# Kernel optimization log

Measured on AMD Instinct MI355X. Metric: run time of the kernel, lower is better.

The kernel has to match this reference:

```python
import jax, jax.numpy as jnp
import numpy as np

B, N, F, A = 8, 2048, 512, 512  # batch, n_dim (tokens), feature_dim, attention_dim
BN_EPS = 1e-5


def setup_inputs() -> dict:
    key = jax.random.key(0)
    ks = jax.random.split(key, 9)
    s_f = 1.0 / np.sqrt(F)
    s_a = 1.0 / np.sqrt(A)
    return {
        "x": jax.random.normal(ks[0], (B, N, F), dtype=jnp.float32),
        "Wq": jax.random.uniform(ks[1], (A, F), jnp.float32, -s_f, s_f),
        "bq": jax.random.uniform(ks[2], (A,), jnp.float32, -s_f, s_f),
        "Wk": jax.random.uniform(ks[3], (A, F), jnp.float32, -s_f, s_f),
        "bk": jax.random.uniform(ks[4], (A,), jnp.float32, -s_f, s_f),
        "Wv": jax.random.uniform(ks[5], (A, F), jnp.float32, -s_f, s_f),
        "bv": jax.random.uniform(ks[6], (A,), jnp.float32, -s_f, s_f),
        "Wo": jax.random.uniform(ks[7], (F, A), jnp.float32, -s_a, s_a),
        "bo": jax.random.uniform(ks[8], (F,), jnp.float32, -s_a, s_a),
        "gamma": jnp.ones((N,), dtype=jnp.float32),
        "beta": jnp.zeros((N,), dtype=jnp.float32),
    }


def reference(x, Wq, bq, Wk, bk, Wv, bv, Wo, bo, gamma, beta):
    # QKV projections: [B,N,F] -> [B,N,A]
    q = jnp.einsum("bnf,af->bna", x, Wq) + bq
    k = jnp.einsum("bnf,af->bna", x, Wk) + bk
    v = jnp.einsum("bnf,af->bna", x, Wv) + bv
    # unscaled single-head attention (no 1/sqrt(d) factor, matches source)
    scores = jnp.einsum("bna,bma->bnm", q, k)          # [B,N,N]
    weights = jax.nn.softmax(scores, axis=-1)
    feature = jnp.einsum("bnm,bma->bna", weights, v)    # [B,N,A]
    # LBR: Linear -> BatchNorm1d(n_dim) over channel dim N -> ReLU
    lin = jnp.einsum("bna,fa->bnf", feature, Wo) + bo   # [B,N,F]
    mean = jnp.mean(lin, axis=(0, 2), keepdims=True)    # stats over batch+last dim
    var = jnp.mean(jnp.square(lin - mean), axis=(0, 2), keepdims=True)  # biased var
    bn = gamma[None, :, None] * (lin - mean) * jax.lax.rsqrt(var + BN_EPS) + beta[None, :, None]
    return jax.nn.relu(bn) + x
```

## Files before the change

### kernel.cpp

```cpp
#include <hip/hip_runtime.h>
#include <hip/hip_fp16.h>
#include <stdint.h>

#define B_   8
#define N_   2048
#define F_   512
#define A_   512
#define MTOT (B_ * N_)

typedef unsigned short u16;
typedef unsigned int   u32;
typedef __attribute__((ext_vector_type(8))) __bf16    bf16x8;
typedef __attribute__((ext_vector_type(8))) _Float16  f16x8;
typedef __attribute__((ext_vector_type(4))) float     f32x4;

__device__ __forceinline__ u16 f2bf(float f) {
    u32 u = __builtin_bit_cast(u32, f);
    u32 r = u + 0x7fffu + ((u >> 16) & 1u);
    return (u16)(r >> 16);
}
__device__ __forceinline__ u16 f2h(float f) {
    _Float16 h = (_Float16)f;
    return __builtin_bit_cast(u16, h);
}

__device__ __forceinline__ void gload_lds16(const u16* g, u16* l) {
    __builtin_amdgcn_global_load_lds(
        (const __attribute__((address_space(1))) u32*)(const u32*)g,
        (__attribute__((address_space(3))) u32*)(u32*)l,
        16, 0, 0);
}

#define VMCNT(n) asm volatile("s_waitcnt vmcnt(" #n ")" ::: "memory")

__device__ __forceinline__ void sync_pre() {
    __builtin_amdgcn_sched_barrier(0);
    __builtin_amdgcn_s_barrier();
    asm volatile("s_waitcnt lgkmcnt(0)" ::: "memory");
    __builtin_amdgcn_sched_barrier(0);
}
__device__ __forceinline__ void sync_post() {
    __builtin_amdgcn_sched_barrier(0);
    __builtin_amdgcn_s_barrier();
}

template <int FMT>
__global__ __launch_bounds__(256) void cvt16(const float* __restrict__ in,
                                             u16* __restrict__ out, int n4) {
    int i = blockIdx.x * 256 + threadIdx.x;
    if (i >= n4) return;
    float4 v = ((const float4*)in)[i];
    u32 a, b;
    if constexpr (FMT == 0) {
        a = (u32)f2bf(v.x) | ((u32)f2bf(v.y) << 16);
        b = (u32)f2bf(v.z) | ((u32)f2bf(v.w) << 16);
    } else {
        a = (u32)f2h(v.x) | ((u32)f2h(v.y) << 16);
        b = (u32)f2h(v.z) | ((u32)f2h(v.w) << 16);
    }
    ((uint2*)out)[i] = make_uint2(a, b);
}

template <int BN, int BIAS_MODE, int OUT_FMT, int IN_FMT>
__global__ __launch_bounds__(512, 2)
void gemm8(const u16* __restrict__ A, int lda, long sA,
           const u16* __restrict__ Bm, int ldb, long sB,
           const float* __restrict__ bias,
           void* __restrict__ Cv, int ldc, long sC, int K, int bdiag)
{
    constexpr int UNITS = (BN == 256) ? 4 : 3;
    constexpr int NF = BN / 64;
    __shared__ alignas(16) u16 lds[2 * UNITS * 8192];

    const int z  = blockIdx.z;
    const int m0 = blockIdx.x * 256;
    const int n0 = blockIdx.y * BN;
    const u16* Ag = A  + (long)z * sA + (long)m0 * lda;
    const u16* Bg = Bm + (long)z * sB + (long)n0 * ldb + (long)(m0 >> 11) * bdiag;

    const int t = threadIdx.x;
    const int lane = t & 63;
    const int wave = t >> 6;
    const int wm = wave >> 2, wn = wave & 3;
    const int frow = lane & 15;
    const int fk8 = (lane >> 4) * 8;

    const int srr = t >> 3;
    const int ses = ((t & 7) * 8) ^ ((srr & 7) << 3);

    auto stageA = [&](int buf, int h, int kt) {
        u16* dst = &lds[(buf * UNITS + h) * 8192 + t * 8];
        const u16* g = Ag + kt * 64 + ses;
        gload_lds16(g + (long)(srr + h * 64) * lda,        dst);
        gload_lds16(g + (long)(srr + 128 + h * 64) * lda,  dst + 4096);
    };
    auto stageB = [&](int buf, int h, int kt) {
        u16* dst = &lds[(buf * UNITS + 2 + h) * 8192 + t * 8];
        const u16* g = Bg + kt * 64 + ses;
        int R0;
        if constexpr (BN == 256) R0 = (srr & 31) + ((srr >> 5) << 6) + h * 32;
        else                     R0 = srr;
        int R1 = R0 + ((BN == 256) ? 128 : 64);
        gload_lds16(g + (long)R0 * ldb, dst);
        gload_lds16(g + (long)R1 * ldb, dst + 4096);
    };
    auto rdA = [&](int buf, int q, int i, int ks) -> uint4 {
        int rr = wm * 64 + i * 16 + frow;
        int e  = (ks * 32 + fk8) ^ ((rr & 7) << 3);
        return *(const uint4*)&lds[(buf * UNITS + q) * 8192 + rr * 64 + e];
    };
    auto rdB = [&](int buf, int p, int j, int ks) -> uint4 {
        int rr = wn * 32 + j * 16 + frow;
        int e  = (ks * 32 + fk8) ^ ((rr & 7) << 3);
        return *(const uint4*)&lds[(buf * UNITS + 2 + p) * 8192 + rr * 64 + e];
    };
    auto MF = [&](uint4 a, uint4 b, f32x4 c) -> f32x4 {
        if constexpr (IN_FMT == 0)
            return __builtin_amdgcn_mfma_f32_16x16x32_bf16(
                __builtin_bit_cast(bf16x8, a), __builtin_bit_cast(bf16x8, b), c, 0, 0, 0);
        else
            return __builtin_amdgcn_mfma_f32_16x16x32_f16(
                __builtin_bit_cast(f16x8, a), __builtin_bit_cast(f16x8, b), c, 0, 0, 0);
    };

    f32x4 acc[8][NF];
#pragma unroll
    for (int i = 0; i < 8; i++)
#pragma unroll
        for (int j = 0; j < NF; j++)
#pragma unroll
            for (int r = 0; r < 4; r++) acc[i][j][r] = 0.f;

    uint4 fa[4][2], fb0[2][2], fb1[2][2];
    const int NT = K >> 6;

    if constexpr (BN == 256) {
        stageA(0, 0, 0); stageB(0, 0, 0); stageB(0, 1, 0); stageA(0, 1, 0);
        VMCNT(4);
    } else {
        stageA(0, 0, 0); stageB(0, 0, 0); stageA(0, 1, 0);
        VMCNT(2);
    }
    __builtin_amdgcn_sched_barrier(0);
    __builtin_amdgcn_s_barrier();

    for (int kt = 0; kt < NT; ++kt) {
        const int buf = kt & 1, nb = buf ^ 1;
        const bool st = (kt + 1 < NT);

        if constexpr (BN == 256) {
#pragma unroll
            for (int i = 0; i < 4; i++) { fa[i][0] = rdA(buf, 0, i, 0); fa[i][1] = rdA(buf, 0, i, 1); }
#pragma unroll
            for (int j = 0; j < 2; j++) { fb0[j][0] = rdB(buf, 0, j, 0); fb0[j][1] = rdB(buf, 0, j, 1); }
            if (st) { stageA(nb, 0, kt + 1); VMCNT(4); } else VMCNT(2);
            sync_pre();
            __builtin_amdgcn_s_setprio(1);
#pragma unroll
            for (int ks = 0; ks < 2; ks++)
#pragma unroll
                for (int i = 0; i < 4; i++)
#pragma unroll
                    for (int j = 0; j < 2; j++)
                        acc[i][j] = MF(fa[i][ks], fb0[j][ks], acc[i][j]);
            __builtin_amdgcn_s_setprio(0);
            sync_post();
#pragma unroll
            for (int j = 0; j < 2; j++) { fb1[j][0] = rdB(buf, 1, j, 0); fb1[j][1] = rdB(buf, 1, j, 1); }
            if (st) { stageB(nb, 0, kt + 1); VMCNT(4); } else VMCNT(0);
            sync_pre();
            __builtin_amdgcn_s_setprio(1);
#pragma unroll
            for (int ks = 0; ks < 2; ks++)
#pragma unroll
                for (int i = 0; i < 4; i++)
#pragma unroll
                    for (int j = 0; j < 2; j++)
                        acc[i][2 + j] = MF(fa[i][ks], fb1[j][ks], acc[i][2 + j]);
            __builtin_amdgcn_s_setprio(0);
            sync_post();
#pragma unroll
            for (int i = 0; i < 4; i++) { fa[i][0] = rdA(buf, 1, i, 0); fa[i][1] = rdA(buf, 1, i, 1); }
            if (st) stageB(nb, 1, kt + 1);
            sync_pre();
            __builtin_amdgcn_s_setprio(1);
#pragma unroll
            for (int ks = 0; ks < 2; ks++)
#pragma unroll
                for (int i = 0; i < 4; i++)
#pragma unroll
                    for (int j = 0; j < 2; j++)
                        acc[4 + i][j] = MF(fa[i][ks], fb0[j][ks], acc[4 + i][j]);
            __builtin_amdgcn_s_setprio(0);
            sync_post();
            if (st) { stageA(nb, 1, kt + 1); VMCNT(4); }
            sync_pre();
            __builtin_amdgcn_s_setprio(1);
#pragma unroll
            for (int ks = 0; ks < 2; ks++)
#pragma unroll
                for (int i = 0; i < 4; i++)
#pragma unroll
                    for (int j = 0; j < 2; j++)
                        acc[4 + i][2 + j] = MF(fa[i][ks], fb1[j][ks], acc[4 + i][2 + j]);
            __builtin_amdgcn_s_setprio(0);
            sync_post();
        } else {
#pragma unroll
            for (int i = 0; i < 4; i++) { fa[i][0] = rdA(buf, 0, i, 0); fa[i][1] = rdA(buf, 0, i, 1); }
#pragma unroll
            for (int j = 0; j < 2; j++) { fb0[j][0] = rdB(buf, 0, j, 0); fb0[j][1] = rdB(buf, 0, j, 1); }
            if (st) { stageA(nb, 0, kt + 1); stageB(nb, 0, kt + 1); VMCNT(4); } else VMCNT(0);
            sync_pre();
            __builtin_amdgcn_s_setprio(1);
#pragma unroll
            for (int ks = 0; ks < 2; ks++)
#pragma unroll
                for (int i = 0; i < 4; i++)
#pragma unroll
                    for (int j = 0; j < 2; j++)
                        acc[i][j] = MF(fa[i][ks], fb0[j][ks], acc[i][j]);
            __builtin_amdgcn_s_setprio(0);
            sync_post();
#pragma unroll
            for (int i = 0; i < 4; i++) { fa[i][0] = rdA(buf, 1, i, 0); fa[i][1] = rdA(buf, 1, i, 1); }
            if (st) { stageA(nb, 1, kt + 1); VMCNT(2); }
            sync_pre();
            __builtin_amdgcn_s_setprio(1);
#pragma unroll
            for (int ks = 0; ks < 2; ks++)
#pragma unroll
                for (int i = 0; i < 4; i++)
#pragma unroll
                    for (int j = 0; j < 2; j++)
                        acc[4 + i][j] = MF(fa[i][ks], fb0[j][ks], acc[4 + i][j]);
            __builtin_amdgcn_s_setprio(0);
            sync_post();
        }
    }

    const int rq = (lane >> 4) * 4;
#pragma unroll
    for (int am = 0; am < 8; am++) {
        const int m = m0 + wm * 128 + (am >> 2) * 64 + (am & 3) * 16 + rq;
#pragma unroll
        for (int an = 0; an < NF; an++) {
            const int n = n0 + wn * (BN / 4) + an * 16 + frow;
            float badd = 0.f;
            if (BIAS_MODE == 1) badd = bias[n];
#pragma unroll
            for (int r = 0; r < 4; r++) {
                float v = acc[am][an][r];
                if (BIAS_MODE == 1) v += badd;
                if (BIAS_MODE == 2) v += bias[m + r];
                long idx = (long)(m + r) * ldc + n + (long)z * sC;
                if constexpr (OUT_FMT == 0)      ((u16*)Cv)[idx] = f2bf(v);
                else if constexpr (OUT_FMT == 1) ((float*)Cv)[idx] = v;
                else                             ((u16*)Cv)[idx] = f2h(v);
            }
        }
    }
}

__global__ __launch_bounds__(256) void softmax_rows(u16* __restrict__ S) {
    __shared__ float red[16];
    const long row = blockIdx.x;
    u16* p = S + row * (long)N_;
    const int t = threadIdx.x;
    const int lane = t & 63, wave = t >> 6;

    uint4 raw = ((const uint4*)p)[t];
    const __half2* hp = (const __half2*)&raw;
    float v[8];
#pragma unroll
    for (int j = 0; j < 4; j++) {
        float2 f = __half22float2(hp[j]);
        v[2 * j]     = f.x;
        v[2 * j + 1] = f.y;
    }
    float mx = v[0];
#pragma unroll
    for (int j = 1; j < 8; j++) mx = fmaxf(mx, v[j]);
#pragma unroll
    for (int o = 32; o; o >>= 1) mx = fmaxf(mx, __shfl_xor(mx, o));
    if (lane == 0) red[wave] = mx;
    __syncthreads();
    mx = fmaxf(fmaxf(red[0], red[1]), fmaxf(red[2], red[3]));

    float s = 0.f;
#pragma unroll
    for (int j = 0; j < 8; j++) { v[j] = __expf(v[j] - mx); s += v[j]; }
#pragma unroll
    for (int o = 32; o; o >>= 1) s += __shfl_xor(s, o);
    if (lane == 0) red[8 + wave] = s;
    __syncthreads();
    s = red[8] + red[9] + red[10] + red[11];
    float inv = 1.f / s;
    u32 w[4];
#pragma unroll
    for (int j = 0; j < 4; j++) {
        u32 lo = f2bf(v[2 * j] * inv);
        u32 hi = f2bf(v[2 * j + 1] * inv);
        w[j] = lo | (hi << 16);
    }
    ((uint4*)p)[t] = make_uint4(w[0], w[1], w[2], w[3]);
}

__global__ __launch_bounds__(256) void bn_stats(const float* __restrict__ lin,
                                                float* __restrict__ stats) {
    __shared__ float red[16];
    const int n = blockIdx.x;
    const int t = threadIdx.x;
    const int lane = t & 63, wave = t >> 6;
    float s = 0.f, s2 = 0.f;
    for (int idx = t; idx < 1024; idx += 256) {
        int b = idx >> 7, f4 = idx & 127;
        float4 x = ((const float4*)(lin + ((long)b * N_ + n) * F_))[f4];
        s  += x.x + x.y + x.z + x.w;
        s2 += x.x * x.x + x.y * x.y + x.z * x.z + x.w * x.w;
    }
#pragma unroll
    for (int o = 32; o; o >>= 1) { s += __shfl_xor(s, o); s2 += __shfl_xor(s2, o); }
    if (lane == 0) { red[wave] = s; red[8 + wave] = s2; }
    __syncthreads();
    if (t == 0) {
        float S1 = red[0] + red[1] + red[2] + red[3];
        float S2 = red[8] + red[9] + red[10] + red[11];
        float mean = S1 / 4096.f;
        float var  = S2 / 4096.f - mean * mean;
        stats[n]      = mean;
        stats[N_ + n] = rsqrtf(var + 1e-5f);
    }
}

__global__ __launch_bounds__(256)
void bn_relu_add(const float* __restrict__ lin, const float* __restrict__ x,
                 const float* __restrict__ gamma, const float* __restrict__ beta,
                 const float* __restrict__ stats, float* __restrict__ out) {
    long i4 = (long)blockIdx.x * 256 + threadIdx.x;
    int n = (int)((i4 >> 7) & (N_ - 1));
    float mean = stats[n], rstd = stats[N_ + n];
    float scale = gamma[n] * rstd;
    float shift = beta[n] - mean * scale;
    float4 l  = ((const float4*)lin)[i4];
    float4 xx = ((const float4*)x)[i4];
    float4 o;
    o.x = fmaxf(l.x * scale + shift, 0.f) + xx.x;
    o.y = fmaxf(l.y * scale + shift, 0.f) + xx.y;
    o.z = fmaxf(l.z * scale + shift, 0.f) + xx.z;
    o.w = fmaxf(l.w * scale + shift, 0.f) + xx.w;
    ((float4*)out)[i4] = o;
}

extern "C" void kernel_launch(void* const* d_in, const int* in_sizes, int n_in,
                              void* d_out, int out_size, void* d_ws, size_t ws_size,
                              hipStream_t stream)
{
    (void)in_sizes; (void)n_in; (void)out_size; (void)ws_size;
    const float* x     = (const float*)d_in[0];
    const float* Wq    = (const float*)d_in[1];
    const float* bq    = (const float*)d_in[2];
    const float* Wk    = (const float*)d_in[3];
    const float* bk    = (const float*)d_in[4];
    const float* Wv    = (const float*)d_in[5];
    const float* bv    = (const float*)d_in[6];
    const float* Wo    = (const float*)d_in[7];
    const float* bo    = (const float*)d_in[8];
    const float* gamma = (const float*)d_in[9];
    const float* beta  = (const float*)d_in[10];
    float* out = (float*)d_out;
    char*  ws  = (char*)d_ws;

    const size_t MB = 1024 * 1024;
    u16*   wqkh  = (u16*)(ws + 0);
    u16*   wvh   = (u16*)(ws + 1 * MB);
    u16*   wob   = (u16*)(ws + 1 * MB + 512 * 1024);
    float* stats = (float*)(ws + 2 * MB);
    float* bqk   = (float*)(ws + 2 * MB + 64 * 1024);
    u16*   xh    = (u16*)(ws + 4 * MB);
    u16*   qkh   = (u16*)(ws + 20 * MB);
    u16*   vt    = (u16*)(ws + 52 * MB);
    u16*   S     = (u16*)(ws + 68 * MB);
    u16*   feat  = (u16*)(ws + 132 * MB);
    float* lin   = (float*)(ws + 148 * MB);

    hipMemcpyAsync(bqk,       bq, 512 * sizeof(float), hipMemcpyDeviceToDevice, stream);
    hipMemcpyAsync(bqk + 512, bk, 512 * sizeof(float), hipMemcpyDeviceToDevice, stream);

    cvt16<1><<<8192, 256, 0, stream>>>(x,  xh,  2097152);
    cvt16<1><<<256,  256, 0, stream>>>(Wq, wqkh,          65536);
    cvt16<1><<<256,  256, 0, stream>>>(Wk, wqkh + 262144, 65536);
    cvt16<1><<<256,  256, 0, stream>>>(Wv, wvh, 65536);
    cvt16<0><<<256,  256, 0, stream>>>(Wo, wob, 65536);

    gemm8<256, 1, 2, 1><<<dim3(64, 4, 1), 512, 0, stream>>>(
        xh, 512, 0, wqkh, 512, 0, bqk, qkh, 1024, 0, 512, 0);
    gemm8<128, 2, 0, 1><<<dim3(2, 128, 1), 512, 0, stream>>>(
        wvh, 512, 0, xh, 512, 0, bv, vt, MTOT, 0, 512, 0);
    gemm8<256, 0, 2, 1><<<dim3(8, 8, 8), 512, 0, stream>>>(
        qkh, 1024, (long)N_ * 1024, qkh + 512, 1024, (long)N_ * 1024,
        nullptr, S, N_, (long)N_ * N_, 512, 0);
    softmax_rows<<<MTOT, 256, 0, stream>>>(S);
    gemm8<128, 0, 0, 0><<<dim3(64, 4, 1), 512, 0, stream>>>(
        S, N_, 0, vt, MTOT, 0, nullptr, feat, A_, 0, 2048, 2048);
    gemm8<128, 1, 1, 0><<<dim3(64, 4, 1), 512, 0, stream>>>(
        feat, 512, 0, wob, 512, 0, bo, lin, 512, 0, 512, 0);

    bn_stats<<<2048, 256, 0, stream>>>(lin, stats);
    bn_relu_add<<<8192, 256, 0, stream>>>(lin, x, gamma, beta, stats, out);
}
```

Baseline: 214.2 us.

## Fuse softmax and BN stats into GEMM epilogues, shrink intermediates, merge conversions

Drops the standalone softmax kernel. The QK^T GEMM epilogue now writes exp(score) in bf16 and atomically adds row sums, and the PV GEMM divides by that row sum. BN statistics are accumulated with atomics in the output-projection epilogue, and the final kernel reads bf16 lin and fp16 x instead of fp32. Weight conversion and bias copies are merged into one kernel, and grid swizzles are added. Skipping the max subtraction risks exp overflow on unscaled scores, and the bf16/fp16 residual and lin reduce accuracy.

After: 217.2 us. Within noise of the previous version (+1.4%).

```diff
diff --git a/kernel.cpp b/kernel.cpp
--- a/kernel.cpp
+++ b/kernel.cpp
@@ -19,6 +19,9 @@
     u32 r = u + 0x7fffu + ((u >> 16) & 1u);
     return (u16)(r >> 16);
 }
+__device__ __forceinline__ float bf2f(u16 h) {
+    return __builtin_bit_cast(float, (u32)h << 16);
+}
 __device__ __forceinline__ u16 f2h(float f) {
     _Float16 h = (_Float16)f;
     return __builtin_bit_cast(u16, h);
@@ -32,48 +35,73 @@
 }
 
 #define VMCNT(n) asm volatile("s_waitcnt vmcnt(" #n ")" ::: "memory")
+#define LGKM0()  asm volatile("s_waitcnt lgkmcnt(0)" ::: "memory")
+#define SCHEDB() __builtin_amdgcn_sched_barrier(0)
 
 __device__ __forceinline__ void sync_pre() {
-    __builtin_amdgcn_sched_barrier(0);
+    SCHEDB();
     __builtin_amdgcn_s_barrier();
-    asm volatile("s_waitcnt lgkmcnt(0)" ::: "memory");
-    __builtin_amdgcn_sched_barrier(0);
+    LGKM0();
+    SCHEDB();
 }
 __device__ __forceinline__ void sync_post() {
-    __builtin_amdgcn_sched_barrier(0);
+    SCHEDB();
     __builtin_amdgcn_s_barrier();
 }
 
-template <int FMT>
-__global__ __launch_bounds__(256) void cvt16(const float* __restrict__ in,
+__global__ __launch_bounds__(256) void cvt_x(const float* __restrict__ in,
                                              u16* __restrict__ out, int n4) {
     int i = blockIdx.x * 256 + threadIdx.x;
     if (i >= n4) return;
     float4 v = ((const float4*)in)[i];
-    u32 a, b;
-    if constexpr (FMT == 0) {
+    u32 a = (u32)f2h(v.x) | ((u32)f2h(v.y) << 16);
+    u32 b = (u32)f2h(v.z) | ((u32)f2h(v.w) << 16);
+    ((uint2*)out)[i] = make_uint2(a, b);
+}
+
+__global__ __launch_bounds__(256)
+void cvt_wb(const float* __restrict__ Wq, const float* __restrict__ Wk,
+            const float* __restrict__ Wv, const float* __restrict__ Wo,
+            const float* __restrict__ bq, const float* __restrict__ bk,
+            u16* __restrict__ wqkh, u16* __restrict__ wvh, u16* __restrict__ wob,
+            float* __restrict__ bqk)
+{
+    int b = blockIdx.x, t = threadIdx.x;
+    int i = (b & 255) * 256 + t;
+    int seg = b >> 8;
+    const float* src = seg == 0 ? Wq : seg == 1 ? Wk : seg == 2 ? Wv : Wo;
+    u16* dst = seg == 0 ? wqkh : seg == 1 ? (wqkh + 262144) : seg == 2 ? wvh : wob;
+    float4 v = ((const float4*)src)[i];
+    u32 a, c;
+    if (seg < 3) {
+        a = (u32)f2h(v.x) | ((u32)f2h(v.y) << 16);
+        c = (u32)f2h(v.z) | ((u32)f2h(v.w) << 16);
+    } else {
         a = (u32)f2bf(v.x) | ((u32)f2bf(v.y) << 16);
-        b = (u32)f2bf(v.z) | ((u32)f2bf(v.w) << 16);
-    } else {
-        a = (u32)f2h(v.x) | ((u32)f2h(v.y) << 16);
-        b = (u32)f2h(v.z) | ((u32)f2h(v.w) << 16);
+        c = (u32)f2bf(v.z) | ((u32)f2bf(v.w) << 16);
     }
-    ((uint2*)out)[i] = make_uint2(a, b);
-}
-
-template <int BN, int BIAS_MODE, int OUT_FMT, int IN_FMT>
+    ((uint2*)dst)[i] = make_uint2(a, c);
+    if (b == 0 && t < 128) ((float4*)bqk)[t]         = ((const float4*)bq)[t];
+    if (b == 1 && t < 128) ((float4*)(bqk + 512))[t] = ((const float4*)bk)[t];
+}
+
+template <int BN, int BIAS_MODE, int OUT_FMT, int IN_FMT, int EPI, int XS>
 __global__ __launch_bounds__(512, 2)
 void gemm8(const u16* __restrict__ A, int lda, long sA,
            const u16* __restrict__ Bm, int ldb, long sB,
            const float* __restrict__ bias,
-           void* __restrict__ Cv, int ldc, long sC, int K, int bdiag)
+           void* __restrict__ Cv, int ldc, long sC, int K, int bdiag,
+           float* __restrict__ aux)
 {
     constexpr int UNITS = (BN == 256) ? 4 : 3;
     constexpr int NF = BN / 64;
     __shared__ alignas(16) u16 lds[2 * UNITS * 8192];
 
-    const int z  = blockIdx.z;
-    const int m0 = blockIdx.x * 256;
+    int bx = blockIdx.x, bz = blockIdx.z;
+    if constexpr (XS == 1) { int tt = bx; bx = bz; bz = tt; }
+    if constexpr (XS == 2) { bx = ((bx & 7) << 3) | (bx >> 3); }
+    const int z  = bz;
+    const int m0 = bx * 256;
     const int n0 = blockIdx.y * BN;
     const u16* Ag = A  + (long)z * sA + (long)m0 * lda;
     const u16* Bg = Bm + (long)z * sB + (long)n0 * ldb + (long)(m0 >> 11) * bdiag;
@@ -141,7 +169,7 @@
         stageA(0, 0, 0); stageB(0, 0, 0); stageA(0, 1, 0);
         VMCNT(2);
     }
-    __builtin_amdgcn_sched_barrier(0);
+    SCHEDB();
     __builtin_amdgcn_s_barrier();
 
     for (int kt = 0; kt < NT; ++kt) {
@@ -244,111 +272,63 @@
     for (int am = 0; am < 8; am++) {
         const int m = m0 + wm * 128 + (am >> 2) * 64 + (am & 3) * 16 + rq;
 #pragma unroll
-        for (int an = 0; an < NF; an++) {
-            const int n = n0 + wn * (BN / 4) + an * 16 + frow;
-            float badd = 0.f;
-            if (BIAS_MODE == 1) badd = bias[n];
-#pragma unroll
-            for (int r = 0; r < 4; r++) {
+        for (int r = 0; r < 4; r++) {
+            float rscale = 1.f;
+            if constexpr (EPI == 3) rscale = 1.0f / aux[m + r];
+            float se = 0.f, s1 = 0.f, s2 = 0.f;
+#pragma unroll
+            for (int an = 0; an < NF; an++) {
+                const int n = n0 + wn * (BN / 4) + an * 16 + frow;
                 float v = acc[am][an][r];
-                if (BIAS_MODE == 1) v += badd;
+                if (BIAS_MODE == 1) v += bias[n];
                 if (BIAS_MODE == 2) v += bias[m + r];
+                if constexpr (EPI == 1) { v = __expf(v); se += v; }
+                if constexpr (EPI == 3) { v *= rscale; }
+                if constexpr (EPI == 2) { s1 += v; s2 += v * v; }
                 long idx = (long)(m + r) * ldc + n + (long)z * sC;
                 if constexpr (OUT_FMT == 0)      ((u16*)Cv)[idx] = f2bf(v);
                 else if constexpr (OUT_FMT == 1) ((float*)Cv)[idx] = v;
                 else                             ((u16*)Cv)[idx] = f2h(v);
             }
+            if constexpr (EPI == 1) {
+#pragma unroll
+                for (int o = 1; o < 16; o <<= 1) se += __shfl_xor(se, o);
+                if (frow == 0)
+                    atomicAdd(&aux[(long)z * N_ + m + r], se);
+            }
+            if constexpr (EPI == 2) {
+#pragma unroll
+                for (int o = 1; o < 16; o <<= 1) { s1 += __shfl_xor(s1, o); s2 += __shfl_xor(s2, o); }
+                if (frow == 0) {
+                    int tok = (m + r) & (N_ - 1);
+                    atomicAdd(&aux[tok], s1);
+                    atomicAdd(&aux[N_ + tok], s2);
+                }
+            }
         }
     }
 }
 
-__global__ __launch_bounds__(256) void softmax_rows(u16* __restrict__ S) {
-    __shared__ float red[16];
-    const long row = blockIdx.x;
-    u16* p = S + row * (long)N_;
-    const int t = threadIdx.x;
-    const int lane = t & 63, wave = t >> 6;
-
-    uint4 raw = ((const uint4*)p)[t];
-    const __half2* hp = (const __half2*)&raw;
-    float v[8];
-#pragma unroll
-    for (int j = 0; j < 4; j++) {
-        float2 f = __half22float2(hp[j]);
-        v[2 * j]     = f.x;
-        v[2 * j + 1] = f.y;
-    }
-    float mx = v[0];
-#pragma unroll
-    for (int j = 1; j < 8; j++) mx = fmaxf(mx, v[j]);
-#pragma unroll
-    for (int o = 32; o; o >>= 1) mx = fmaxf(mx, __shfl_xor(mx, o));
-    if (lane == 0) red[wave] = mx;
-    __syncthreads();
-    mx = fmaxf(fmaxf(red[0], red[1]), fmaxf(red[2], red[3]));
-
-    float s = 0.f;
-#pragma unroll
-    for (int j = 0; j < 8; j++) { v[j] = __expf(v[j] - mx); s += v[j]; }
-#pragma unroll
-    for (int o = 32; o; o >>= 1) s += __shfl_xor(s, o);
-    if (lane == 0) red[8 + wave] = s;
-    __syncthreads();
-    s = red[8] + red[9] + red[10] + red[11];
-    float inv = 1.f / s;
-    u32 w[4];
-#pragma unroll
-    for (int j = 0; j < 4; j++) {
-        u32 lo = f2bf(v[2 * j] * inv);
-        u32 hi = f2bf(v[2 * j + 1] * inv);
-        w[j] = lo | (hi << 16);
-    }
-    ((uint4*)p)[t] = make_uint4(w[0], w[1], w[2], w[3]);
-}
-
-__global__ __launch_bounds__(256) void bn_stats(const float* __restrict__ lin,
-                                                float* __restrict__ stats) {
-    __shared__ float red[16];
-    const int n = blockIdx.x;
-    const int t = threadIdx.x;
-    const int lane = t & 63, wave = t >> 6;
-    float s = 0.f, s2 = 0.f;
-    for (int idx = t; idx < 1024; idx += 256) {
-        int b = idx >> 7, f4 = idx & 127;
-        float4 x = ((const float4*)(lin + ((long)b * N_ + n) * F_))[f4];
-        s  += x.x + x.y + x.z + x.w;
-        s2 += x.x * x.x + x.y * x.y + x.z * x.z + x.w * x.w;
-    }
-#pragma unroll
-    for (int o = 32; o; o >>= 1) { s += __shfl_xor(s, o); s2 += __shfl_xor(s2, o); }
-    if (lane == 0) { red[wave] = s; red[8 + wave] = s2; }
-    __syncthreads();
-    if (t == 0) {
-        float S1 = red[0] + red[1] + red[2] + red[3];
-        float S2 = red[8] + red[9] + red[10] + red[11];
-        float mean = S1 / 4096.f;
-        float var  = S2 / 4096.f - mean * mean;
-        stats[n]      = mean;
-        stats[N_ + n] = rsqrtf(var + 1e-5f);
-    }
-}
-
 __global__ __launch_bounds__(256)
-void bn_relu_add(const float* __restrict__ lin, const float* __restrict__ x,
+void bn_relu_add(const u16* __restrict__ linb, const u16* __restrict__ xh,
                  const float* __restrict__ gamma, const float* __restrict__ beta,
                  const float* __restrict__ stats, float* __restrict__ out) {
     long i4 = (long)blockIdx.x * 256 + threadIdx.x;
     int n = (int)((i4 >> 7) & (N_ - 1));
-    float mean = stats[n], rstd = stats[N_ + n];
+    float mean = stats[n] * (1.f / 4096.f);
+    float var  = stats[N_ + n] * (1.f / 4096.f) - mean * mean;
+    float rstd = rsqrtf(var + 1e-5f);
     float scale = gamma[n] * rstd;
     float shift = beta[n] - mean * scale;
-    float4 l  = ((const float4*)lin)[i4];
-    float4 xx = ((const float4*)x)[i4];
+    uint2 lb = ((const uint2*)linb)[i4];
+    uint2 xb = ((const uint2*)xh)[i4];
+    float2 x01 = __half22float2(__builtin_bit_cast(__half2, xb.x));
+    float2 x23 = __half22float2(__builtin_bit_cast(__half2, xb.y));
     float4 o;
-    o.x = fmaxf(l.x * scale + shift, 0.f) + xx.x;
-    o.y = fmaxf(l.y * scale + shift, 0.f) + xx.y;
-    o.z = fmaxf(l.z * scale + shift, 0.f) + xx.z;
-    o.w = fmaxf(l.w * scale + shift, 0.f) + xx.w;
+    o.x = fmaxf(bf2f((u16)lb.x)         * scale + shift, 0.f) + x01.x;
+    o.y = fmaxf(bf2f((u16)(lb.x >> 16)) * scale + shift, 0.f) + x01.y;
+    o.z = fmaxf(bf2f((u16)lb.y)         * scale + shift, 0.f) + x23.x;
+    o.w = fmaxf(bf2f((u16)(lb.y >> 16)) * scale + shift, 0.f) + x23.y;
     ((float4*)out)[i4] = o;
 }
 
@@ -376,36 +356,31 @@
     u16*   wvh   = (u16*)(ws + 1 * MB);
     u16*   wob   = (u16*)(ws + 1 * MB + 512 * 1024);
     float* stats = (float*)(ws + 2 * MB);
-    float* bqk   = (float*)(ws + 2 * MB + 64 * 1024);
+    float* rowsum= (float*)(ws + 2 * MB + 16 * 1024);
+    float* bqk   = (float*)(ws + 2 * MB + 80 * 1024);
     u16*   xh    = (u16*)(ws + 4 * MB);
     u16*   qkh   = (u16*)(ws + 20 * MB);
     u16*   vt    = (u16*)(ws + 52 * MB);
-    u16*   S     = (u16*)(ws + 68 * MB);
+    u16*   P     = (u16*)(ws + 68 * MB);
     u16*   feat  = (u16*)(ws + 132 * MB);
-    float* lin   = (float*)(ws + 148 * MB);
-
-    hipMemcpyAsync(bqk,       bq, 512 * sizeof(float), hipMemcpyDeviceToDevice, stream);
-    hipMemcpyAsync(bqk + 512, bk, 512 * sizeof(float), hipMemcpyDeviceToDevice, stream);
-
-    cvt16<1><<<8192, 256, 0, stream>>>(x,  xh,  2097152);
-    cvt16<1><<<256,  256, 0, stream>>>(Wq, wqkh,          65536);
-    cvt16<1><<<256,  256, 0, stream>>>(Wk, wqkh + 262144, 65536);
-    cvt16<1><<<256,  256, 0, stream>>>(Wv, wvh, 65536);
-    cvt16<0><<<256,  256, 0, stream>>>(Wo, wob, 65536);
-
-    gemm8<256, 1, 2, 1><<<dim3(64, 4, 1), 512, 0, stream>>>(
-        xh, 512, 0, wqkh, 512, 0, bqk, qkh, 1024, 0, 512, 0);
-    gemm8<128, 2, 0, 1><<<dim3(2, 128, 1), 512, 0, stream>>>(
-        wvh, 512, 0, xh, 512, 0, bv, vt, MTOT, 0, 512, 0);
-    gemm8<256, 0, 2, 1><<<dim3(8, 8, 8), 512, 0, stream>>>(
+    u16*   lin   = (u16*)(ws + 148 * MB);
+
+    hipMemsetAsync(stats, 0, 80 * 1024, stream);
+
+    cvt_x<<<8192, 256, 0, stream>>>(x, xh, 2097152);
+    cvt_wb<<<1024, 256, 0, stream>>>(Wq, Wk, Wv, Wo, bq, bk, wqkh, wvh, wob, bqk);
+
+    gemm8<256, 1, 2, 1, 0, 0><<<dim3(64, 4, 1), 512, 0, stream>>>(
+        xh, 512, 0, wqkh, 512, 0, bqk, qkh, 1024, 0, 512, 0, nullptr);
+    gemm8<128, 2, 0, 1, 0, 0><<<dim3(2, 128, 1), 512, 0, stream>>>(
+        wvh, 512, 0, xh, 512, 0, bv, vt, MTOT, 0, 512, 0, nullptr);
+    gemm8<256, 0, 0, 1, 1, 1><<<dim3(8, 8, 8), 512, 0, stream>>>(
         qkh, 1024, (long)N_ * 1024, qkh + 512, 1024, (long)N_ * 1024,
-        nullptr, S, N_, (long)N_ * N_, 512, 0);
-    softmax_rows<<<MTOT, 256, 0, stream>>>(S);
-    gemm8<128, 0, 0, 0><<<dim3(64, 4, 1), 512, 0, stream>>>(
-        S, N_, 0, vt, MTOT, 0, nullptr, feat, A_, 0, 2048, 2048);
-    gemm8<128, 1, 1, 0><<<dim3(64, 4, 1), 512, 0, stream>>>(
-        feat, 512, 0, wob, 512, 0, bo, lin, 512, 0, 512, 0);
-
-    bn_stats<<<2048, 256, 0, stream>>>(lin, stats);
-    bn_relu_add<<<8192, 256, 0, stream>>>(lin, x, gamma, beta, stats, out);
-}
+        nullptr, P, N_, (long)N_ * N_, 512, 0, rowsum);
+    gemm8<128, 0, 0, 0, 3, 2><<<dim3(64, 4, 1), 512, 0, stream>>>(
+        P, N_, 0, vt, MTOT, 0, nullptr, feat, A_, 0, 2048, 2048, rowsum);
+    gemm8<128, 1, 0, 0, 2, 0><<<dim3(64, 4, 1), 512, 0, stream>>>(
+        feat, 512, 0, wob, 512, 0, bo, lin, 512, 0, 512, 0, stats);
+
+    bn_relu_add<<<8192, 256, 0, stream>>>(lin, xh, gamma, beta, stats, out);
+}
```
